# Kernel optimization log

Hardware: AMD Instinct MI355X
Metric: run time of the kernel (lower is better)

The kernel has to match this reference:

```python
import jax, jax.numpy as jnp
import numpy as np

# module hyperparameters (match init_kwargs)
D_IN = 32
N_BAND_IN = 32
D_OUT = 32
K_BAND = 4
K_T = 3
DIL_T = 1
STRIDE_B = 2
PAD_B = 1
PAD_B_OUT = 0

# derived band geometry (same formulas as ConvTranspose2dBandPadder)
N_UP = (N_BAND_IN - 1) * STRIDE_B + 1            # zero-interleaved bands
PAD_TOP = K_BAND - 1 - PAD_B
PAD_BOT = PAD_TOP + PAD_B_OUT
N_PADDED = N_UP + PAD_TOP + PAD_BOT              # bands fed to the conv
N_BAND_OUT = N_PADDED - K_BAND + 1               # valid conv along bands

B = 8
T = 1000


def setup_inputs() -> dict:
    key = jax.random.key(0)
    k1, k2, k3 = jax.random.split(key, 3)
    x = jax.random.normal(k1, (B, D_IN * N_BAND_IN, T), jnp.float32)
    W = jax.random.normal(k2, (D_OUT, D_IN, K_BAND, K_T), jnp.float32) * 0.05
    b = jax.random.normal(k3, (D_OUT,), jnp.float32) * 0.05
    return {"x": x, "W": W, "b": b}


def reference(x, W, b):
    """x: (B, D_IN*N_BAND_IN, T) band-major channels -> (B, D_OUT*N_BAND_OUT, T)."""
    Bs, _, Ts = x.shape
    # chunk(dim=1, n_band_in): band-major layout (band, feature)
    bands = x.reshape(Bs, N_BAND_IN, D_IN, Ts)
    # zero-interleave bands by stride + top/bottom zero-band padding
    up = jnp.zeros((Bs, N_PADDED, D_IN, Ts), x.dtype)
    up = up.at[:, PAD_TOP:PAD_TOP + N_UP:STRIDE_B].set(bands)
    # 2D conv: channels = D_IN, spatial = (band, time), causal in time
    xin = up.transpose(0, 2, 1, 3)  # (B, D_IN, N_PADDED, T)
    pad_t = (K_T - 1) * DIL_T
    y = jax.lax.conv_general_dilated(
        xin, W,
        window_strides=(1, 1),
        padding=((0, 0), (pad_t, 0)),  # valid over bands, causal over time
        rhs_dilation=(1, DIL_T),
        dimension_numbers=("NCHW", "OIHW", "NCHW"),
    )  # (B, D_OUT, N_BAND_OUT, T)
    y = y + b[None, :, None, None]
    # back to band-major flattened channels
    return y.transpose(0, 2, 1, 3).reshape(Bs, D_OUT * N_BAND_OUT, Ts)
```

## Files before the change

### kernel.cpp

```cpp
#include <hip/hip_runtime.h>
#include <cstddef>
#include <cstdint>


typedef __bf16 bf16x8 __attribute__((ext_vector_type(8)));
typedef __bf16 bf16x4 __attribute__((ext_vector_type(4)));
typedef float  f32x4  __attribute__((ext_vector_type(4)));

#define D_IN_ 32
#define D_OUT_ 32
#define N_BI_ 32
#define N_BO_ 64
#define K_B_ 4
#define K_T_ 3
#define T_ 1000
#define B_ 8

#define TT_ 256
#define XT_ 260
#define ROWB_ 64
#define WT_ELEMS (2 * 6 * 2 * 64 * 8)

__device__ __forceinline__ int swz(int t) { return (t & 3) ^ ((t >> 2) & 3); }

__global__ __launch_bounds__(256)
void wprep(const float* __restrict__ W, __bf16* __restrict__ wt) {
    int idx = blockIdx.x * 256 + threadIdx.x;
    if (idx >= WT_ELEMS) return;
    int r = idx & 7, l = (idx >> 3) & 63, mt = (idx >> 9) & 1, rest = idx >> 10;
    int ks = rest % 6, p = rest / 6;
    int dout = mt * 16 + (l & 15), din = (l >> 4) * 8 + r;
    int j = ks / 3, kt = ks % 3, kb = 2 * j + p;
    wt[idx] = (__bf16)W[((dout * D_IN_ + din) * K_B_ + kb) * K_T_ + kt];
}

__global__ __launch_bounds__(256, 3)
void tct_mfma(const float* __restrict__ x, const __bf16* __restrict__ wt,
              const float* __restrict__ bias, float* __restrict__ out)
{
    __shared__ unsigned char xl[2 * XT_ * ROWB_];

    const int tid = threadIdx.x;
    const int l   = tid & 63;
    const int w   = tid >> 6;
    const int n   = blockIdx.y;
    const int bb  = blockIdx.z;
    const int p   = n & 1, q = n >> 1;
    const int t0  = blockIdx.x * TT_;
    const int tstart = t0 - 4;

    bf16x8 afrag[6][2];
    {
        const bf16x8* wp = (const bf16x8*)wt;
        const int base = p * 12 * 64;
#pragma unroll
        for (int ks = 0; ks < 6; ++ks)
#pragma unroll
            for (int mt = 0; mt < 2; ++mt)
                afrag[ks][mt] = wp[base + (ks * 2 + mt) * 64 + l];
    }

    {
        const int u  = tid & 15;
        const int si = u >> 3;
        const int dg = u & 7;
        const int s  = q + si + p - 1;
        const bool bandok = (s >= 0) && (s < N_BI_);
        const float* xb = x + ((size_t)(bb * N_BI_ + (bandok ? s : 0)) * D_IN_ + dg * 4) * T_;
        unsigned char* lbase = xl + si * (XT_ * ROWB_);
        const int c = dg >> 1, h = dg & 1;
        for (int tq = (tid >> 4); tq < XT_ / 4; tq += 16) {
            const int tg = tstart + tq * 4;
            float vv[4][4];
            if (bandok && tg >= 0 && tg < T_) {
#pragma unroll
                for (int i = 0; i < 4; ++i)
                    *(float4*)&vv[i][0] = *(const float4*)(xb + (size_t)i * T_ + tg);
            } else {
#pragma unroll
                for (int i = 0; i < 4; ++i)
#pragma unroll
                    for (int k = 0; k < 4; ++k) vv[i][k] = 0.f;
            }
#pragma unroll
            for (int k = 0; k < 4; ++k) {
                const int t = tq * 4 + k;
                bf16x4 row;
                row[0] = (__bf16)vv[0][k];
                row[1] = (__bf16)vv[1][k];
                row[2] = (__bf16)vv[2][k];
                row[3] = (__bf16)vv[3][k];
                *(bf16x4*)(lbase + t * ROWB_ + ((c ^ swz(t)) << 4) + (h << 3)) = row;
            }
        }
    }
    __syncthreads();

    f32x4 acc[2][4];
#pragma unroll
    for (int mt = 0; mt < 2; ++mt)
#pragma unroll
        for (int nt = 0; nt < 4; ++nt)
#pragma unroll
            for (int r = 0; r < 4; ++r) acc[mt][nt][r] = 0.f;

    const int tl = (l & 15);
    const int cch = l >> 4;
#pragma unroll
    for (int nt = 0; nt < 4; ++nt) {
#pragma unroll
        for (int ks = 0; ks < 6; ++ks) {
            const int j  = ks / 3, kt = ks % 3;
            const int lt = w * 64 + nt * 16 + tl + kt + 2;
            const bf16x8 bfrag = *(const bf16x8*)(xl + j * (XT_ * ROWB_) + lt * ROWB_
                                                  + ((cch ^ swz(lt)) << 4));
            acc[0][nt] = __builtin_amdgcn_mfma_f32_16x16x32_bf16(afrag[ks][0], bfrag, acc[0][nt], 0, 0, 0);
            acc[1][nt] = __builtin_amdgcn_mfma_f32_16x16x32_bf16(afrag[ks][1], bfrag, acc[1][nt], 0, 0, 0);
        }
    }

    const int rbase = (l >> 4) * 4;
    float bv[2][4];
#pragma unroll
    for (int mt = 0; mt < 2; ++mt)
#pragma unroll
        for (int r = 0; r < 4; ++r) bv[mt][r] = bias[mt * 16 + rbase + r];

#pragma unroll
    for (int mt = 0; mt < 2; ++mt)
#pragma unroll
        for (int nt = 0; nt < 4; ++nt) {
            const int tcol = t0 + w * 64 + nt * 16 + tl;
            if (tcol < T_) {
                float* op = out + ((size_t)(bb * N_BO_ + n) * D_OUT_ + mt * 16 + rbase) * T_ + tcol;
#pragma unroll
                for (int r = 0; r < 4; ++r)
                    op[(size_t)r * T_] = acc[mt][nt][r] + bv[mt][r];
            }
        }
}

__global__ __launch_bounds__(256)
void tct_fallback(const float* __restrict__ x, const float* __restrict__ W,
                  const float* __restrict__ bias, float* __restrict__ out)
{
    const int lane = threadIdx.x & 63;
    const int wav  = __builtin_amdgcn_readfirstlane(threadIdx.x >> 6);
    const int dog  = wav * 8;
    const int n    = blockIdx.y;
    const int bb   = blockIdx.z;
    const int p    = n & 1;

    int t0 = blockIdx.x * 256 + lane * 4;
    const bool act = (t0 < T_);
    if (!act) t0 = T_ - 4;

    float acc[8][4];
#pragma unroll
    for (int i = 0; i < 8; ++i)
#pragma unroll
        for (int u = 0; u < 4; ++u) acc[i][u] = 0.f;

#pragma unroll
    for (int j = 0; j < 2; ++j) {
        const int s = (n + 2 * j + p - 2) >> 1;
        if (s < 0 || s >= N_BI_) continue;
        const int kb = 2 * j + p;
        const float* xband = x + (size_t)(bb * N_BI_ + s) * D_IN_ * T_;
        for (int d_in = 0; d_in < D_IN_; ++d_in) {
            const float* xr = xband + d_in * T_;
            const float4 xc = *(const float4*)(xr + t0);
            float4 xp = make_float4(0.f, 0.f, 0.f, 0.f);
            if (t0 > 0) xp = *(const float4*)(xr + t0 - 4);
            const float xv[6] = {xp.z, xp.w, xc.x, xc.y, xc.z, xc.w};
#pragma unroll
            for (int kt = 0; kt < K_T_; ++kt) {
                float wv[8];
#pragma unroll
                for (int i = 0; i < 8; ++i) {
                    const int widx = __builtin_amdgcn_readfirstlane(
                        (((dog + i) * D_IN_ + d_in) * K_B_ + kb) * K_T_ + kt);
                    wv[i] = W[widx];
                }
#pragma unroll
                for (int i = 0; i < 8; ++i)
#pragma unroll
                    for (int u = 0; u < 4; ++u)
                        acc[i][u] = fmaf(wv[i], xv[u + kt], acc[i][u]);
            }
        }
    }
    if (act) {
        float bvv[8];
#pragma unroll
        for (int i = 0; i < 8; ++i) bvv[i] = bias[dog + i];
        float* op = out + ((size_t)(bb * N_BO_ + n) * D_OUT_ + dog) * T_ + t0;
#pragma unroll
        for (int i = 0; i < 8; ++i) {
            float4 v;
            v.x = acc[i][0] + bvv[i];
            v.y = acc[i][1] + bvv[i];
            v.z = acc[i][2] + bvv[i];
            v.w = acc[i][3] + bvv[i];
            *(float4*)(op + (size_t)i * T_) = v;
        }
    }
}

extern "C" void kernel_launch(void* const* d_in, const int* in_sizes, int n_in,
                              void* d_out, int out_size, void* d_ws, size_t ws_size,
                              hipStream_t stream) {
    const float* x    = (const float*)d_in[0];
    const float* W    = (const float*)d_in[1];
    const float* bias = (const float*)d_in[2];
    float* out = (float*)d_out;

    dim3 grid((T_ + TT_ - 1) / TT_, N_BO_, B_);
    dim3 block(256);

    if (ws_size >= (size_t)WT_ELEMS * sizeof(__bf16)) {
        __bf16* wt = (__bf16*)d_ws;
        wprep<<<(WT_ELEMS + 255) / 256, 256, 0, stream>>>(W, wt);
        tct_mfma<<<grid, block, 0, stream>>>(x, wt, bias, out);
    } else {
        tct_fallback<<<grid, block, 0, stream>>>(x, W, bias, out);
    }
}
```

Measured before the change: 115.0 us.

## Use 512-thread blocks with 8 waves and batch global loads before LDS stores

Doubles the block to 512 threads, so each of 8 waves computes 32 time columns instead of 64. The time tile shrinks to 252 so the 256 staged rows cover the causal halo. The staging loop now issues both iterations' global float4 loads before any bf16 LDS writes, and staggers the per-thread write order to spread LDS bank accesses. The aim is more memory-level parallelism and better latency hiding; the cost is a slightly redundant halo per tile and a changed occupancy and register budget.

```diff
diff --git a/kernel.cpp b/kernel.cpp
--- a/kernel.cpp
+++ b/kernel.cpp
@@ -16,8 +16,8 @@
 #define T_ 1000
 #define B_ 8
 
-#define TT_ 256
-#define XT_ 260
+#define TT_ 252
+#define XROWS_ 260
 #define ROWB_ 64
 #define WT_ELEMS (2 * 6 * 2 * 64 * 8)
 
@@ -34,11 +34,11 @@
     wt[idx] = (__bf16)W[((dout * D_IN_ + din) * K_B_ + kb) * K_T_ + kt];
 }
 
-__global__ __launch_bounds__(256, 3)
+__global__ __launch_bounds__(512, 4)
 void tct_mfma(const float* __restrict__ x, const __bf16* __restrict__ wt,
               const float* __restrict__ bias, float* __restrict__ out)
 {
-    __shared__ unsigned char xl[2 * XT_ * ROWB_];
+    __shared__ unsigned char xl[2 * XROWS_ * ROWB_];
 
     const int tid = threadIdx.x;
     const int l   = tid & 63;
@@ -61,58 +61,66 @@
     }
 
     {
+        const int g  = tid >> 4;
         const int u  = tid & 15;
         const int si = u >> 3;
         const int dg = u & 7;
         const int s  = q + si + p - 1;
         const bool bandok = (s >= 0) && (s < N_BI_);
         const float* xb = x + ((size_t)(bb * N_BI_ + (bandok ? s : 0)) * D_IN_ + dg * 4) * T_;
-        unsigned char* lbase = xl + si * (XT_ * ROWB_);
+        unsigned char* lbase = xl + si * (XROWS_ * ROWB_);
         const int c = dg >> 1, h = dg & 1;
-        for (int tq = (tid >> 4); tq < XT_ / 4; tq += 16) {
+
+        f32x4 vv[2][4];
+        bool ok[2];
+        int tgs[2];
+#pragma unroll
+        for (int it = 0; it < 2; ++it) {
+            const int tq = g + it * 32;
             const int tg = tstart + tq * 4;
-            float vv[4][4];
-            if (bandok && tg >= 0 && tg < T_) {
-#pragma unroll
-                for (int i = 0; i < 4; ++i)
-                    *(float4*)&vv[i][0] = *(const float4*)(xb + (size_t)i * T_ + tg);
-            } else {
-#pragma unroll
-                for (int i = 0; i < 4; ++i)
-#pragma unroll
-                    for (int k = 0; k < 4; ++k) vv[i][k] = 0.f;
-            }
-#pragma unroll
-            for (int k = 0; k < 4; ++k) {
+            tgs[it] = tg;
+            ok[it] = bandok && (tg >= 0) && (tg < T_);
+#pragma unroll
+            for (int i = 0; i < 4; ++i) {
+                if (ok[it]) vv[it][i] = *(const f32x4*)(xb + (size_t)i * T_ + tg);
+                else        vv[it][i] = (f32x4){0.f, 0.f, 0.f, 0.f};
+            }
+        }
+#pragma unroll
+        for (int it = 0; it < 2; ++it) {
+            const int tq = g + it * 32;
+#pragma unroll
+            for (int jj = 0; jj < 4; ++jj) {
+                const int k = (jj + g) & 3;
                 const int t = tq * 4 + k;
                 bf16x4 row;
-                row[0] = (__bf16)vv[0][k];
-                row[1] = (__bf16)vv[1][k];
-                row[2] = (__bf16)vv[2][k];
-                row[3] = (__bf16)vv[3][k];
+                row[0] = (__bf16)vv[it][0][k];
+                row[1] = (__bf16)vv[it][1][k];
+                row[2] = (__bf16)vv[it][2][k];
+                row[3] = (__bf16)vv[it][3][k];
                 *(bf16x4*)(lbase + t * ROWB_ + ((c ^ swz(t)) << 4) + (h << 3)) = row;
             }
         }
     }
     __syncthreads();
 
-    f32x4 acc[2][4];
+    f32x4 acc[2][2];
 #pragma unroll
     for (int mt = 0; mt < 2; ++mt)
 #pragma unroll
-        for (int nt = 0; nt < 4; ++nt)
+        for (int nt = 0; nt < 2; ++nt)
 #pragma unroll
             for (int r = 0; r < 4; ++r) acc[mt][nt][r] = 0.f;
 
-    const int tl = (l & 15);
+    const int tl  = l & 15;
     const int cch = l >> 4;
 #pragma unroll
-    for (int nt = 0; nt < 4; ++nt) {
+    for (int nt = 0; nt < 2; ++nt) {
 #pragma unroll
         for (int ks = 0; ks < 6; ++ks) {
             const int j  = ks / 3, kt = ks % 3;
-            const int lt = w * 64 + nt * 16 + tl + kt + 2;
-            const bf16x8 bfrag = *(const bf16x8*)(xl + j * (XT_ * ROWB_) + lt * ROWB_
+            const int lt = w * 32 + nt * 16 + tl + kt + 2;
+            const bf16x8 bfrag = *(const bf16x8*)(xl + j * (XROWS_ * ROWB_) + lt * ROWB_
                                                   + ((cch ^ swz(lt)) << 4));
             acc[0][nt] = __builtin_amdgcn_mfma_f32_16x16x32_bf16(afrag[ks][0], bfrag, acc[0][nt], 0, 0, 0);
             acc[1][nt] = __builtin_amdgcn_mfma_f32_16x16x32_bf16(afrag[ks][1], bfrag, acc[1][nt], 0, 0, 0);
@@ -129,9 +137,10 @@
 #pragma unroll
     for (int mt = 0; mt < 2; ++mt)
 #pragma unroll
-        for (int nt = 0; nt < 4; ++nt) {
-            const int tcol = t0 + w * 64 + nt * 16 + tl;
-            if (tcol < T_) {
+        for (int nt = 0; nt < 2; ++nt) {
+            const int lcol = w * 32 + nt * 16 + tl;
+            const int tcol = t0 + lcol;
+            if (lcol < TT_ && tcol < T_) {
                 float* op = out + ((size_t)(bb * N_BO_ + n) * D_OUT_ + mt * 16 + rbase) * T_ + tcol;
 #pragma unroll
                 for (int r = 0; r < 4; ++r)
@@ -215,14 +224,13 @@
     const float* bias = (const float*)d_in[2];
     float* out = (float*)d_out;
 
-    dim3 grid((T_ + TT_ - 1) / TT_, N_BO_, B_);
-    dim3 block(256);
-
     if (ws_size >= (size_t)WT_ELEMS * sizeof(__bf16)) {
         __bf16* wt = (__bf16*)d_ws;
         wprep<<<(WT_ELEMS + 255) / 256, 256, 0, stream>>>(W, wt);
-        tct_mfma<<<grid, block, 0, stream>>>(x, wt, bias, out);
+        dim3 grid((T_ + TT_ - 1) / TT_, N_BO_, B_);
+        tct_mfma<<<grid, dim3(512), 0, stream>>>(x, wt, bias, out);
     } else {
-        tct_fallback<<<grid, block, 0, stream>>>(x, W, bias, out);
-    }
-}
+        dim3 grid((T_ + 255) / 256, N_BO_, B_);
+        tct_fallback<<<grid, dim3(256), 0, stream>>>(x, W, bias, out);
+    }
+}
```

After: 120.7 us. 4.9% more time.
